# Kernel optimization log

Hardware: AMD Instinct MI355X
Metric: run time of the kernel (lower is better)

Reference implementation:

```python
import jax, jax.numpy as jnp
import numpy as np

N = 50000      # nodes
E = 400000     # edges (before self-loops)
IN = 128
HID = 64
HEADS = 8
OUT = 3
NEG_SLOPE = 0.2
EPS = 1e-6


def setup_inputs() -> dict:
    key = jax.random.key(0)
    ks = jax.random.split(key, 32)
    def nrm(k, shape, s=0.05):
        return jax.random.normal(k, shape, dtype=jnp.float32) * s
    inp = {}
    inp['x'] = nrm(ks[0], (N, IN), 1.0)
    inp['edge_index'] = jax.random.randint(ks[1], (2, E), 0, N)
    inp['res_W'] = nrm(ks[2], (OUT, IN))
    inp['res_b'] = jnp.zeros((OUT,), jnp.float32)
    # (in, out, heads, concat) per GAT layer
    dims = [(IN, HID, HEADS, True), (HID * HEADS, HID, HEADS, True),
            (HID * HEADS, HID, HEADS, True), (HID * HEADS, OUT, 1, False)]
    j = 3
    for i, (ci, co, h, cc) in enumerate(dims):
        inp['ln_g%d' % i] = jnp.ones((ci,), jnp.float32)
        inp['ln_b%d' % i] = jnp.zeros((ci,), jnp.float32)
        inp['W%d' % i] = nrm(ks[j], (h * co, ci)); j += 1
        inp['asr%d' % i] = nrm(ks[j], (h, co)); j += 1
        inp['adt%d' % i] = nrm(ks[j], (h, co)); j += 1
        inp['b%d' % i] = jnp.zeros((h * co if cc else co,), jnp.float32)
    return inp


def layer_norm(x, g, b):
    mu = x.mean(-1, keepdims=True)
    var = ((x - mu) ** 2).mean(-1, keepdims=True)
    return (x - mu) / jnp.sqrt(var + EPS) * g + b


def gat_conv(x, src, dst, W, a_src, a_dst, bias, heads, co, concat):
    n = x.shape[0]
    h = (x @ W.T).reshape(n, heads, co)                    # [N,H,C]
    al_src = jnp.sum(h * a_src, axis=-1)                   # [N,H]
    al_dst = jnp.sum(h * a_dst, axis=-1)                   # [N,H]
    e = jax.nn.leaky_relu(al_src[src] + al_dst[dst], NEG_SLOPE)  # [E',H]
    # segment softmax over incoming edges of each destination node
    m = jax.ops.segment_max(e, dst, num_segments=n)
    e = jnp.exp(e - m[dst])
    s = jax.ops.segment_sum(e, dst, num_segments=n)
    alpha = e / s[dst]                                     # [E',H]
    msg = h[src] * alpha[..., None]                        # [E',H,C]
    out = jax.ops.segment_sum(msg, dst, num_segments=n)    # [N,H,C]
    out = out.reshape(n, heads * co) if concat else out.mean(axis=1)
    return out + bias


def reference(x, edge_index, res_W, res_b,
              ln_g0, ln_b0, W0, asr0, adt0, b0,
              ln_g1, ln_b1, W1, asr1, adt1, b1,
              ln_g2, ln_b2, W2, asr2, adt2, b2,
              ln_g3, ln_b3, W3, asr3, adt3, b3):
    n = x.shape[0]
    loops = jnp.arange(n)
    src = jnp.concatenate([edge_index[0], loops])          # add self-loops (PyG default)
    dst = jnp.concatenate([edge_index[1], loops])
    residual = x @ res_W.T + res_b
    layers = [(ln_g0, ln_b0, W0, asr0, adt0, b0, HEADS, HID, True),
              (ln_g1, ln_b1, W1, asr1, adt1, b1, HEADS, HID, True),
              (ln_g2, ln_b2, W2, asr2, adt2, b2, HEADS, HID, True),
              (ln_g3, ln_b3, W3, asr3, adt3, b3, 1, OUT, False)]
    h = x
    num_layers = len(layers)
    for i, (g, bb, W, a_s, a_d, bi, hd, co, cc) in enumerate(layers):
        x_res = h
        h = layer_norm(h, g, bb)
        h = gat_conv(h, src, dst, W, a_s, a_d, bi, hd, co, cc)
        if i < num_layers - 1:
            h = jax.nn.gelu(h, approximate=False)
            if h.shape == x_res.shape:
                h = h + x_res
    return h + residual
```

## Files before the change

### kernel.cpp

```cpp
#include <hip/hip_runtime.h>
#include <math.h>

#define NN 50000
#define MPAD 50048
#define EE 400000
#define NE 450000
#define IN_F 128
#define NEG_SLOPE 0.2f
#define EPSV 1e-6f

typedef unsigned short bf16u;
typedef short bf8_t __attribute__((ext_vector_type(8)));
typedef float f32x4 __attribute__((ext_vector_type(4)));

__device__ __forceinline__ float bf2f(unsigned int u) {
    return __uint_as_float(u << 16);
}
__device__ __forceinline__ float bf2f_hi(unsigned int u) {
    return __uint_as_float(u & 0xFFFF0000u);
}
__device__ __forceinline__ bf16u f2bf(float f) {
    unsigned int u = __float_as_uint(f);
    unsigned int r = (u + 0x7FFFu + ((u >> 16) & 1u)) >> 16;
    return (bf16u)r;
}
__device__ __forceinline__ float gelu_f(float v) {
    return 0.5f * v * (1.0f + erff(v * 0.70710678118654752f));
}

__device__ __forceinline__ void gload_lds16(const void* g, void* l) {
    __builtin_amdgcn_global_load_lds(
        (__attribute__((address_space(1))) void*)(g),
        (__attribute__((address_space(3))) void*)(l), 16, 0, 0);
}

__global__ void k_zero_i32(int* p, int n) {
    int i = blockIdx.x * 256 + threadIdx.x;
    if (i < n) p[i] = 0;
}

__global__ void k_deg(const int* __restrict__ ei, int* __restrict__ deg) {
    int i = blockIdx.x * 256 + threadIdx.x;
    if (i >= NE) return;
    int d = (i < EE) ? ei[EE + i] : (i - EE);
    atomicAdd(&deg[d], 1);
}

__global__ __launch_bounds__(256) void k_scan1(const int* __restrict__ deg,
                                               int* __restrict__ incl,
                                               int* __restrict__ bsums, int n) {
    __shared__ int sm[1024];
    int base = blockIdx.x * 1024;
    for (int i = threadIdx.x; i < 1024; i += 256)
        sm[i] = (base + i < n) ? deg[base + i] : 0;
    __syncthreads();
    for (int off = 1; off < 1024; off <<= 1) {
        int v[4];
#pragma unroll
        for (int j = 0; j < 4; j++) {
            int i = threadIdx.x + 256 * j;
            v[j] = (i >= off) ? sm[i - off] : 0;
        }
        __syncthreads();
#pragma unroll
        for (int j = 0; j < 4; j++) {
            int i = threadIdx.x + 256 * j;
            sm[i] += v[j];
        }
        __syncthreads();
    }
    for (int i = threadIdx.x; i < 1024; i += 256)
        if (base + i < n) incl[base + i] = sm[i];
    if (threadIdx.x == 0) bsums[blockIdx.x] = sm[1023];
}

__global__ void k_scan2(int* bsums, int nb) {
    if (threadIdx.x == 0 && blockIdx.x == 0) {
        int run = 0;
        for (int i = 0; i < nb; i++) { int v = bsums[i]; bsums[i] = run; run += v; }
    }
}

__global__ void k_scan3(const int* __restrict__ deg, int* __restrict__ rowptr,
                        int* __restrict__ cursor, const int* __restrict__ bsums,
                        int n, int ne) {
    int i = blockIdx.x * 256 + threadIdx.x;
    if (i < n) {
        int excl = rowptr[i] + bsums[i >> 10] - deg[i];
        rowptr[i] = excl;
        cursor[i] = excl;
    }
    if (i == n) rowptr[n] = ne;
}

__global__ void k_scatter(const int* __restrict__ ei, int* __restrict__ cursor,
                          int* __restrict__ col) {
    int i = blockIdx.x * 256 + threadIdx.x;
    if (i >= NE) return;
    int s, d;
    if (i < EE) { s = ei[i]; d = ei[EE + i]; }
    else        { s = i - EE; d = i - EE; }
    int p = atomicAdd(&cursor[d], 1);
    col[p] = s;
}

__global__ void k_cast(const float* __restrict__ x, bf16u* __restrict__ h, int total) {
    int i = blockIdx.x * 256 + threadIdx.x;
    if (i < total) h[i] = f2bf(x[i]);
}

__global__ __launch_bounds__(256) void k_castres(const float* __restrict__ x,
                                                 const float* __restrict__ rw,
                                                 const float* __restrict__ rb,
                                                 bf16u* __restrict__ h,
                                                 float* __restrict__ stats,
                                                 float* __restrict__ res, int n) {
    int row = (blockIdx.x * 256 + threadIdx.x) >> 6;
    int lane = threadIdx.x & 63;
    if (row >= n) return;
    float2 v = *(const float2*)(x + (size_t)row * 128 + lane * 2);
    unsigned int pk = (unsigned int)f2bf(v.x) | ((unsigned int)f2bf(v.y) << 16);
    *(unsigned int*)(h + (size_t)row * 128 + lane * 2) = pk;
    float2 w0 = *(const float2*)(rw + 0 * 128 + lane * 2);
    float2 w1 = *(const float2*)(rw + 1 * 128 + lane * 2);
    float2 w2 = *(const float2*)(rw + 2 * 128 + lane * 2);
    float s = v.x + v.y, s2 = v.x * v.x + v.y * v.y;
    float a0 = v.x * w0.x + v.y * w0.y;
    float a1 = v.x * w1.x + v.y * w1.y;
    float a2 = v.x * w2.x + v.y * w2.y;
#pragma unroll
    for (int off = 32; off; off >>= 1) {
        s  += __shfl_xor(s, off);
        s2 += __shfl_xor(s2, off);
        a0 += __shfl_xor(a0, off);
        a1 += __shfl_xor(a1, off);
        a2 += __shfl_xor(a2, off);
    }
    if (lane == 0) {
        float mu = s * (1.0f / 128.0f);
        float var = s2 * (1.0f / 128.0f) - mu * mu;
        stats[row * 2 + 0] = mu;
        stats[row * 2 + 1] = rsqrtf(var + EPSV);
        res[row * 3 + 0] = a0 + rb[0];
        res[row * 3 + 1] = a1 + rb[1];
        res[row * 3 + 2] = a2 + rb[2];
    }
}

#define BM 128
#define BN 128
#define BKK 32
__global__ __launch_bounds__(256) void k_gemm_mfma(const bf16u* __restrict__ H,
                                                   const float* __restrict__ stats,
                                                   const float* __restrict__ g,
                                                   const float* __restrict__ bbias,
                                                   const bf16u* __restrict__ Wb,
                                                   bf16u* __restrict__ C,
                                                   const float* __restrict__ asr,
                                                   const float* __restrict__ adt,
                                                   float* __restrict__ alsrc,
                                                   float* __restrict__ aldst,
                                                   int Mreal, int ci, int K) {
    __shared__ __align__(16) bf16u As[BM * BKK];
    __shared__ __align__(16) bf16u Bs[BN * BKK];
    const int tid = threadIdx.x;
    const int w = tid >> 6, lane = tid & 63;
    const int row0 = blockIdx.x * BM, col0 = blockIdx.y * BN;
    const int wr = (w >> 1) * 64, wc = (w & 1) * 64;

    const int srow = w * 32 + (lane >> 2);
    const int scol = (lane & 3) * 8;
    const bf16u* gA = H + (size_t)(row0 + srow) * ci + scol;
    const bf16u* gB = Wb + (size_t)(col0 + srow) * ci + scol;
    const float mu1 = stats[(row0 + srow) * 2 + 0];
    const float rs1 = stats[(row0 + srow) * 2 + 1];
    const float mu2 = stats[(row0 + srow + 16) * 2 + 0];
    const float rs2 = stats[(row0 + srow + 16) * 2 + 1];
    bf16u* lA1 = &As[(size_t)srow * BKK + scol];
    bf16u* lA2 = &As[(size_t)(srow + 16) * BKK + scol];
    void* lB1 = &Bs[(size_t)(w * 32) * BKK];
    void* lB2 = &Bs[(size_t)(w * 32 + 16) * BKK];

    f32x4 acc[4][4] = {};

    const int fr = lane & 15;
    const int fk = (lane >> 4) * 8;

    for (int k0 = 0; k0 < ci; k0 += BKK) {
        uint4 ra1 = *(const uint4*)(gA + k0);
        uint4 ra2 = *(const uint4*)(gA + (size_t)16 * ci + k0);
        float4 g0 = *(const float4*)(g + k0 + scol);
        float4 g1 = *(const float4*)(g + k0 + scol + 4);
        float4 b0 = *(const float4*)(bbias + k0 + scol);
        float4 b1 = *(const float4*)(bbias + k0 + scol + 4);
        float gg[8] = {g0.x, g0.y, g0.z, g0.w, g1.x, g1.y, g1.z, g1.w};
        float bb[8] = {b0.x, b0.y, b0.z, b0.w, b1.x, b1.y, b1.z, b1.w};
        unsigned int u1[4] = {ra1.x, ra1.y, ra1.z, ra1.w};
        unsigned int u2[4] = {ra2.x, ra2.y, ra2.z, ra2.w};
        uint4 p1, p2;
        {
            unsigned int po[4], qo[4];
#pragma unroll
            for (int j = 0; j < 4; j++) {
                float va = (bf2f(u1[j] & 0xFFFFu) - mu1) * rs1;
                float vb = (bf2f_hi(u1[j])         - mu1) * rs1;
                float oa = fmaf(va, gg[2 * j], bb[2 * j]);
                float ob = fmaf(vb, gg[2 * j + 1], bb[2 * j + 1]);
                po[j] = (unsigned int)f2bf(oa) | ((unsigned int)f2bf(ob) << 16);
                float vc = (bf2f(u2[j] & 0xFFFFu) - mu2) * rs2;
                float vd = (bf2f_hi(u2[j])         - mu2) * rs2;
                float oc = fmaf(vc, gg[2 * j], bb[2 * j]);
                float od = fmaf(vd, gg[2 * j + 1], bb[2 * j + 1]);
                qo[j] = (unsigned int)f2bf(oc) | ((unsigned int)f2bf(od) << 16);
            }
            p1 = make_uint4(po[0], po[1], po[2], po[3]);
            p2 = make_uint4(qo[0], qo[1], qo[2], qo[3]);
        }

        __syncthreads();
        *(uint4*)lA1 = p1;
        *(uint4*)lA2 = p2;
        gload_lds16(gB + k0, lB1);
        gload_lds16(gB + (size_t)16 * ci + k0, lB2);
        __syncthreads();

        bf8_t af[4], bf[4];
#pragma unroll
        for (int m = 0; m < 4; m++)
            af[m] = *(const bf8_t*)&As[(size_t)(wr + m * 16 + fr) * BKK + fk];
#pragma unroll
        for (int n = 0; n < 4; n++)
            bf[n] = *(const bf8_t*)&Bs[(size_t)(wc + n * 16 + fr) * BKK + fk];
#pragma unroll
        for (int m = 0; m < 4; m++)
#pragma unroll
            for (int n = 0; n < 4; n++)
                acc[m][n] = __builtin_amdgcn_mfma_f32_16x16x32_bf16(af[m], bf[n], acc[m][n], 0, 0, 0);
    }

    const int fc = lane & 15;
    const int fq = (lane >> 4) * 4;

#pragma unroll
    for (int m = 0; m < 4; m++) {
#pragma unroll
        for (int r = 0; r < 4; r++) {
            int row = row0 + wr + m * 16 + fq + r;
            if (row >= Mreal) continue;
#pragma unroll
            for (int n = 0; n < 4; n++) {
                int col = col0 + wc + n * 16 + fc;
                C[(size_t)row * K + col] = f2bf(acc[m][n][r]);
            }
        }
    }

    const int head = blockIdx.y * 2 + (wc >> 6);
    float av[4], dv[4];
#pragma unroll
    for (int n = 0; n < 4; n++) {
        av[n] = asr[head * 64 + n * 16 + fc];
        dv[n] = adt[head * 64 + n * 16 + fc];
    }
#pragma unroll
    for (int m = 0; m < 4; m++) {
#pragma unroll
        for (int r = 0; r < 4; r++) {
            float s1 = acc[m][0][r] * av[0] + acc[m][1][r] * av[1]
                     + acc[m][2][r] * av[2] + acc[m][3][r] * av[3];
            float s2 = acc[m][0][r] * dv[0] + acc[m][1][r] * dv[1]
                     + acc[m][2][r] * dv[2] + acc[m][3][r] * dv[3];
#pragma unroll
            for (int o = 1; o < 16; o <<= 1) {
                s1 += __shfl_xor(s1, o);
                s2 += __shfl_xor(s2, o);
            }
            int row = row0 + wr + m * 16 + fq + r;
            if (fc == 0 && row < Mreal) {
                alsrc[row * 8 + head] = s1;
                aldst[row * 8 + head] = s2;
            }
        }
    }
}

__global__ __launch_bounds__(256) void k_lin3(const bf16u* __restrict__ h,
                                              const float* __restrict__ stats,
                                              const float* __restrict__ g,
                                              const float* __restrict__ bb,
                                              const float* __restrict__ W,
                                              const float* __restrict__ a_s,
                                              const float* __restrict__ a_d,
                                              bf16u* __restrict__ hlin3,
                                              float* __restrict__ alsrc,
                                              float* __restrict__ aldst, int n) {
    int row = (blockIdx.x * 256 + threadIdx.x) >> 6;
    int lane = threadIdx.x & 63;
    if (row >= n) return;
    float mu = stats[row * 2 + 0], rs = stats[row * 2 + 1];
    uint4 r = *(const uint4*)(h + (size_t)row * 512 + lane * 8);
    float4 g0 = *(const float4*)(g + lane * 8);
    float4 g1 = *(const float4*)(g + lane * 8 + 4);
    float4 b0 = *(const float4*)(bb + lane * 8);
    float4 b1 = *(const float4*)(bb + lane * 8 + 4);
    float gg[8] = {g0.x, g0.y, g0.z, g0.w, g1.x, g1.y, g1.z, g1.w};
    float bv[8] = {b0.x, b0.y, b0.z, b0.w, b1.x, b1.y, b1.z, b1.w};
    unsigned int u[4] = {r.x, r.y, r.z, r.w};
    float ln[8];
#pragma unroll
    for (int j = 0; j < 4; j++) {
        ln[2 * j]     = fmaf((bf2f(u[j] & 0xFFFFu) - mu) * rs, gg[2 * j], bv[2 * j]);
        ln[2 * j + 1] = fmaf((bf2f_hi(u[j])         - mu) * rs, gg[2 * j + 1], bv[2 * j + 1]);
    }
    float a0 = 0.f, a1 = 0.f, a2 = 0.f;
#pragma unroll
    for (int j = 0; j < 8; j++) {
        int k = lane * 8 + j;
        a0 += ln[j] * W[k];
        a1 += ln[j] * W[512 + k];
        a2 += ln[j] * W[1024 + k];
    }
#pragma unroll
    for (int off = 32; off; off >>= 1) {
        a0 += __shfl_down(a0, off);
        a1 += __shfl_down(a1, off);
        a2 += __shfl_down(a2, off);
    }
    if (lane == 0) {
        *(unsigned int*)(hlin3 + (size_t)row * 4) =
            (unsigned int)f2bf(a0) | ((unsigned int)f2bf(a1) << 16);
        *(unsigned int*)(hlin3 + (size_t)row * 4 + 2) = (unsigned int)f2bf(a2);
        alsrc[row] = a0 * a_s[0] + a1 * a_s[1] + a2 * a_s[2];
        aldst[row] = a0 * a_d[0] + a1 * a_d[1] + a2 * a_d[2];
    }
}

__global__ __launch_bounds__(256) void k_aggN(const bf16u* __restrict__ hlin,
                                              const float* __restrict__ alsrc,
                                              const float* __restrict__ aldst,
                                              const int* __restrict__ rowptr,
                                              const int* __restrict__ col,
                                              const float* __restrict__ bias,
                                              bf16u* __restrict__ hio,
                                              float* __restrict__ stats,
                                              int n, int dores) {
    __shared__ uint2 aldsU[4][8][66];
    int wv = threadIdx.x >> 6;
    int node = (blockIdx.x * 256 + threadIdx.x) >> 6;
    int lane = threadIdx.x & 63;
    if (node >= n) return;
    int beg = rowptr[node], end = rowptr[node + 1];
    int deg = end - beg;

    const float4* dvv = (const float4*)(aldst + node * 8);
    float4 da = dvv[0], db = dvv[1];
    float ad[8] = {da.x, da.y, da.z, da.w, db.x, db.y, db.z, db.w};

    float s = 0.f, s2 = 0.f;

    if (deg <= 64) {
        unsigned int offb = 0;
        float raw[8];
#pragma unroll
        for (int h = 0; h < 8; h++) raw[h] = -INFINITY;
        if (lane < deg) {
            int srcreg = col[beg + lane];
            offb = (unsigned int)srcreg << 10;
            const float4* sv = (const float4*)(alsrc + srcreg * 8);
            float4 sa = sv[0], sb = sv[1];
            float sl[8] = {sa.x, sa.y, sa.z, sa.w, sb.x, sb.y, sb.z, sb.w};
#pragma unroll
            for (int h = 0; h < 8; h++) {
                float v = sl[h] + ad[h];
                raw[h] = (v >= 0.f) ? v : NEG_SLOPE * v;
            }
        }
        float m[8];
#pragma unroll
        for (int h = 0; h < 8; h++) m[h] = raw[h];
#pragma unroll
        for (int off = 32; off; off >>= 1)
#pragma unroll
            for (int h = 0; h < 8; h++) m[h] = fmaxf(m[h], __shfl_xor(m[h], off));
        float ex[8], sm[8];
#pragma unroll
        for (int h = 0; h < 8; h++) {
            ex[h] = (lane < deg) ? __expf(raw[h] - m[h]) : 0.f;
            sm[h] = ex[h];
        }
#pragma unroll
        for (int off = 32; off; off >>= 1)
#pragma unroll
            for (int h = 0; h < 8; h++) sm[h] += __shfl_xor(sm[h], off);
#pragma unroll
        for (int h = 0; h < 8; h++) {
            uint2 t;
            t.x = __float_as_uint(ex[h] * (1.0f / sm[h]));
            t.y = offb;
            aldsU[wv][h][lane] = t;
        }
        asm volatile("s_waitcnt lgkmcnt(0)" ::: "memory");

        int hl = lane >> 3;
        const uint2* myal = &aldsU[wv][hl][0];
        const char* base2 = (const char*)hlin + (lane << 4);
        float acc[8] = {};
        int e = 0;
        for (; e + 2 <= deg; e += 2) {
            uint2 t0 = myal[e];
            uint2 t1 = myal[e + 1];
            uint4 u0 = *(const uint4*)(base2 + t0.y);
            uint4 u1 = *(const uint4*)(base2 + t1.y);
            float a0 = __uint_as_float(t0.x), a1 = __uint_as_float(t1.x);
            acc[0] = fmaf(a0, bf2f(u0.x & 0xFFFFu), acc[0]);
            acc[1] = fmaf(a0, bf2f_hi(u0.x),        acc[1]);
            acc[2] = fmaf(a0, bf2f(u0.y & 0xFFFFu), acc[2]);
            acc[3] = fmaf(a0, bf2f_hi(u0.y),        acc[3]);
            acc[4] = fmaf(a0, bf2f(u0.z & 0xFFFFu), acc[4]);
            acc[5] = fmaf(a0, bf2f_hi(u0.z),        acc[5]);
            acc[6] = fmaf(a0, bf2f(u0.w & 0xFFFFu), acc[6]);
            acc[7] = fmaf(a0, bf2f_hi(u0.w),        acc[7]);
            acc[0] = fmaf(a1, bf2f(u1.x & 0xFFFFu), acc[0]);
            acc[1] = fmaf(a1, bf2f_hi(u1.x),        acc[1]);
            acc[2] = fmaf(a1, bf2f(u1.y & 0xFFFFu), acc[2]);
            acc[3] = fmaf(a1, bf2f_hi(u1.y),        acc[3]);
            acc[4] = fmaf(a1, bf2f(u1.z & 0xFFFFu), acc[4]);
            acc[5] = fmaf(a1, bf2f_hi(u1.z),        acc[5]);
            acc[6] = fmaf(a1, bf2f(u1.w & 0xFFFFu), acc[6]);
            acc[7] = fmaf(a1, bf2f_hi(u1.w),        acc[7]);
        }
        if (e < deg) {
            uint2 t0 = myal[e];
            uint4 u0 = *(const uint4*)(base2 + t0.y);
            float a0 = __uint_as_float(t0.x);
            acc[0] = fmaf(a0, bf2f(u0.x & 0xFFFFu), acc[0]);
            acc[1] = fmaf(a0, bf2f_hi(u0.x),        acc[1]);
            acc[2] = fmaf(a0, bf2f(u0.y & 0xFFFFu), acc[2]);
            acc[3] = fmaf(a0, bf2f_hi(u0.y),        acc[3]);
            acc[4] = fmaf(a0, bf2f(u0.z & 0xFFFFu), acc[4]);
            acc[5] = fmaf(a0, bf2f_hi(u0.z),        acc[5]);
            acc[6] = fmaf(a0, bf2f(u0.w & 0xFFFFu), acc[6]);
            acc[7] = fmaf(a0, bf2f_hi(u0.w),        acc[7]);
        }

        size_t idx = (size_t)node * 512 + lane * 8;
        float4 b0 = *(const float4*)(bias + lane * 8);
        float4 b1 = *(const float4*)(bias + lane * 8 + 4);
        float bb[8] = {b0.x, b0.y, b0.z, b0.w, b1.x, b1.y, b1.z, b1.w};
        float fin[8];
#pragma unroll
        for (int j = 0; j < 8; j++) fin[j] = gelu_f(acc[j] + bb[j]);
        if (dores) {
            uint4 up = *(const uint4*)(hio + idx);
            fin[0] += bf2f(up.x & 0xFFFFu); fin[1] += bf2f_hi(up.x);
            fin[2] += bf2f(up.y & 0xFFFFu); fin[3] += bf2f_hi(up.y);
            fin[4] += bf2f(up.z & 0xFFFFu); fin[5] += bf2f_hi(up.z);
            fin[6] += bf2f(up.w & 0xFFFFu); fin[7] += bf2f_hi(up.w);
        }
        uint4 pk;
        pk.x = (unsigned int)f2bf(fin[0]) | ((unsigned int)f2bf(fin[1]) << 16);
        pk.y = (unsigned int)f2bf(fin[2]) | ((unsigned int)f2bf(fin[3]) << 16);
        pk.z = (unsigned int)f2bf(fin[4]) | ((unsigned int)f2bf(fin[5]) << 16);
        pk.w = (unsigned int)f2bf(fin[6]) | ((unsigned int)f2bf(fin[7]) << 16);
        *(uint4*)(hio + idx) = pk;
#pragma unroll
        for (int j = 0; j < 8; j++) { s += fin[j]; s2 += fin[j] * fin[j]; }
    } else {
        for (int h = 0; h < 8; h++) {
            float adh = ad[h];
            float m = -INFINITY;
            for (int e = beg + lane; e < end; e += 64) {
                float v = alsrc[col[e] * 8 + h] + adh;
                v = (v >= 0.f) ? v : NEG_SLOPE * v;
                m = fmaxf(m, v);
            }
#pragma unroll
            for (int off = 32; off; off >>= 1) m = fmaxf(m, __shfl_xor(m, off));
            float sum = 0.f;
            for (int e = beg + lane; e < end; e += 64) {
                float v = alsrc[col[e] * 8 + h] + adh;
                v = (v >= 0.f) ? v : NEG_SLOPE * v;
                sum += __expf(v - m);
            }
#pragma unroll
            for (int off = 32; off; off >>= 1) sum += __shfl_xor(sum, off);
            float inv = 1.0f / sum;
            float acc = 0.f;
            for (int e = beg; e < end; e++) {
                int src = col[e];
                float v = alsrc[src * 8 + h] + adh;
                v = (v >= 0.f) ? v : NEG_SLOPE * v;
                float alpha = __expf(v - m) * inv;
                acc = fmaf(alpha, bf2f(hlin[((size_t)src << 9) + h * 64 + lane]), acc);
            }
            float fin = gelu_f(acc + bias[h * 64 + lane]);
            size_t idx = (size_t)node * 512 + h * 64 + lane;
            if (dores) fin += bf2f(hio[idx]);
            hio[idx] = f2bf(fin);
            s += fin; s2 += fin * fin;
        }
    }

#pragma unroll
    for (int off = 32; off; off >>= 1) {
        s  += __shfl_xor(s, off);
        s2 += __shfl_xor(s2, off);
    }
    if (lane == 0) {
        float mu = s * (1.0f / 512.0f);
        float var = s2 * (1.0f / 512.0f) - mu * mu;
        stats[node * 2 + 0] = mu;
        stats[node * 2 + 1] = rsqrtf(var + EPSV);
    }
}

__global__ __launch_bounds__(256) void k_aggF(const bf16u* __restrict__ hlin3,
                                              const float* __restrict__ alsrc,
                                              const float* __restrict__ aldst,
                                              const int* __restrict__ rowptr,
                                              const int* __restrict__ col,
                                              const float* __restrict__ bias,
                                              float* __restrict__ outf,
                                              const float* __restrict__ resid, int n) {
    int node = (blockIdx.x * 256 + threadIdx.x) >> 6;
    int lane = threadIdx.x & 63;
    if (node >= n) return;
    int beg = rowptr[node], end = rowptr[node + 1];
    int deg = end - beg;
    float adh = aldst[node];

    if (deg <= 64) {
        int src = 0;
        float raw = -INFINITY;
        if (lane < deg) {
            src = col[beg + lane];
            float v = alsrc[src] + adh;
            raw = (v >= 0.f) ? v : NEG_SLOPE * v;
        }
        float m = raw;
#pragma unroll
        for (int off = 32; off; off >>= 1) m = fmaxf(m, __shfl_xor(m, off));
        float ex = (lane < deg) ? __expf(raw - m) : 0.f;
        float sum = ex;
#pragma unroll
        for (int off = 32; off; off >>= 1) sum += __shfl_xor(sum, off);
        float alpha = ex / sum;

        float c0 = 0.f, c1 = 0.f, c2 = 0.f;
        if (lane < deg) {
            uint2 u = *(const uint2*)(hlin3 + (size_t)src * 4);
            c0 = alpha * bf2f(u.x & 0xFFFFu);
            c1 = alpha * bf2f_hi(u.x);
            c2 = alpha * bf2f(u.y & 0xFFFFu);
        }
#pragma unroll
        for (int off = 32; off; off >>= 1) {
            c0 += __shfl_xor(c0, off);
            c1 += __shfl_xor(c1, off);
            c2 += __shfl_xor(c2, off);
        }
        if (lane == 0) {
            outf[node * 3 + 0] = c0 + bias[0] + resid[node * 3 + 0];
            outf[node * 3 + 1] = c1 + bias[1] + resid[node * 3 + 1];
            outf[node * 3 + 2] = c2 + bias[2] + resid[node * 3 + 2];
        }
    } else {
        float m = -INFINITY;
        for (int e = beg + lane; e < end; e += 64) {
            float v = alsrc[col[e]] + adh;
            v = (v >= 0.f) ? v : NEG_SLOPE * v;
            m = fmaxf(m, v);
        }
#pragma unroll
        for (int off = 32; off; off >>= 1) m = fmaxf(m, __shfl_xor(m, off));
        float sum = 0.f;
        for (int e = beg + lane; e < end; e += 64) {
            float v = alsrc[col[e]] + adh;
            v = (v >= 0.f) ? v : NEG_SLOPE * v;
            sum += __expf(v - m);
        }
#pragma unroll
        for (int off = 32; off; off >>= 1) sum += __shfl_xor(sum, off);
        float inv = 1.0f / sum;
        float acc = 0.f;
        for (int e = beg; e < end; e++) {
            int src = col[e];
            float v = alsrc[src] + adh;
            v = (v >= 0.f) ? v : NEG_SLOPE * v;
            float alpha = __expf(v - m) * inv;
            if (lane < 3) acc += alpha * bf2f(hlin3[(size_t)src * 4 + lane]);
        }
        if (lane < 3)
            outf[node * 3 + lane] = acc + bias[lane] + resid[node * 3 + lane];
    }
}

extern "C" void kernel_launch(void* const* d_in, const int* in_sizes, int n_in,
                              void* d_out, int out_size, void* d_ws, size_t ws_size,
                              hipStream_t stream) {
    const float* x    = (const float*)d_in[0];
    const int*   ei   = (const int*)d_in[1];
    const float* resW = (const float*)d_in[2];
    const float* resb = (const float*)d_in[3];
    const float *lng[4], *lnb[4], *Wm[4], *asr[4], *adt[4], *bias[4];
    int idx = 4;
    for (int i = 0; i < 4; i++) {
        lng[i]  = (const float*)d_in[idx++];
        lnb[i]  = (const float*)d_in[idx++];
        Wm[i]   = (const float*)d_in[idx++];
        asr[i]  = (const float*)d_in[idx++];
        adt[i]  = (const float*)d_in[idx++];
        bias[i] = (const float*)d_in[idx++];
    }

    char* base = (char*)d_ws;
    size_t off = 0;
    auto alloc = [&](size_t bytes) {
        void* p = base + off;
        off += (bytes + 255) & ~(size_t)255;
        return p;
    };
    bf16u* hbuf  = (bf16u*)alloc((size_t)MPAD * 512 * 2);
    bf16u* lbuf  = (bf16u*)alloc((size_t)MPAD * 512 * 2);
    bf16u* wb0   = (bf16u*)alloc((size_t)512 * 128 * 2);
    bf16u* wb1   = (bf16u*)alloc((size_t)512 * 512 * 2);
    bf16u* wb2   = (bf16u*)alloc((size_t)512 * 512 * 2);
    float* stats = (float*)alloc((size_t)MPAD * 2 * 4);
    float* alsrc = (float*)alloc((size_t)NN * 8 * 4);
    float* aldst = (float*)alloc((size_t)NN * 8 * 4);
    float* resid = (float*)alloc((size_t)NN * 3 * 4);
    int* rowptr  = (int*)alloc((size_t)(NN + 1) * 4);
    int* cursor  = (int*)alloc((size_t)NN * 4);
    int* deg     = (int*)alloc((size_t)NN * 4);
    int* colidx  = (int*)alloc((size_t)NE * 4);
    int* bsums   = (int*)alloc(256 * 4);
    if (off > ws_size) return;

    float* out = (float*)d_out;

    k_zero_i32<<<(NN + 255) / 256, 256, 0, stream>>>(deg, NN);
    k_deg<<<(NE + 255) / 256, 256, 0, stream>>>(ei, deg);
    int nb = (NN + 1023) / 1024;
    k_scan1<<<nb, 256, 0, stream>>>(deg, rowptr, bsums, NN);
    k_scan2<<<1, 64, 0, stream>>>(bsums, nb);
    k_scan3<<<(NN + 1 + 255) / 256, 256, 0, stream>>>(deg, rowptr, cursor, bsums, NN, NE);
    k_scatter<<<(NE + 255) / 256, 256, 0, stream>>>(ei, cursor, colidx);

    int rowBlocks = (NN * 64 + 255) / 256;
    k_castres<<<rowBlocks, 256, 0, stream>>>(x, resW, resb, hbuf, stats, resid, NN);
    k_cast<<<(512 * 128 + 255) / 256, 256, 0, stream>>>(Wm[0], wb0, 512 * 128);
    k_cast<<<(512 * 512 + 255) / 256, 256, 0, stream>>>(Wm[1], wb1, 512 * 512);
    k_cast<<<(512 * 512 + 255) / 256, 256, 0, stream>>>(Wm[2], wb2, 512 * 512);

    const bf16u* wb[3] = {wb0, wb1, wb2};
    const int ci_a[3] = {128, 512, 512};

    for (int i = 0; i < 3; i++) {
        int ci = ci_a[i];
        int dores = (i >= 1) ? 1 : 0;

        dim3 ggrid(MPAD / BM, 512 / BN);
        k_gemm_mfma<<<ggrid, 256, 0, stream>>>(hbuf, stats, lng[i], lnb[i], wb[i],
                                               lbuf, asr[i], adt[i], alsrc, aldst,
                                               NN, ci, 512);

        k_aggN<<<rowBlocks, 256, 0, stream>>>(lbuf, alsrc, aldst, rowptr, colidx,
                                              bias[i], hbuf, stats, NN, dores);
    }

    k_lin3<<<rowBlocks, 256, 0, stream>>>(hbuf, stats, lng[3], lnb[3], Wm[3],
                                          asr[3], adt[3], lbuf, alsrc, aldst, NN);
    k_aggF<<<rowBlocks, 256, 0, stream>>>(lbuf, alsrc, aldst, rowptr, colidx,
                                          bias[3], out, resid, NN);
}
```

Before: 670.1 us.

## Move LayerNorm into aggregation epilogue and use pure swizzled bf16 GEMM

```diff
diff --git a/kernel.cpp b/kernel.cpp
--- a/kernel.cpp
+++ b/kernel.cpp
@@ -141,6 +141,48 @@
         float var = s2 * (1.0f / 128.0f) - mu * mu;
         stats[row * 2 + 0] = mu;
         stats[row * 2 + 1] = rsqrtf(var + EPSV);
+        res[row * 3 + 0] = a0 + rb[0];
+        res[row * 3 + 1] = a1 + rb[1];
+        res[row * 3 + 2] = a2 + rb[2];
+    }
+}
+
+__global__ __launch_bounds__(256) void k_castres2(const float* __restrict__ x,
+                                                  const float* __restrict__ rw,
+                                                  const float* __restrict__ rb,
+                                                  const float* __restrict__ g0,
+                                                  const float* __restrict__ b0,
+                                                  bf16u* __restrict__ abuf,
+                                                  float* __restrict__ res, int n) {
+    int row = (blockIdx.x * 256 + threadIdx.x) >> 6;
+    int lane = threadIdx.x & 63;
+    if (row >= n) return;
+    float2 v = *(const float2*)(x + (size_t)row * 128 + lane * 2);
+    float2 w0 = *(const float2*)(rw + 0 * 128 + lane * 2);
+    float2 w1 = *(const float2*)(rw + 1 * 128 + lane * 2);
+    float2 w2 = *(const float2*)(rw + 2 * 128 + lane * 2);
+    float s = v.x + v.y, s2 = v.x * v.x + v.y * v.y;
+    float a0 = v.x * w0.x + v.y * w0.y;
+    float a1 = v.x * w1.x + v.y * w1.y;
+    float a2 = v.x * w2.x + v.y * w2.y;
+#pragma unroll
+    for (int off = 32; off; off >>= 1) {
+        s  += __shfl_xor(s, off);
+        s2 += __shfl_xor(s2, off);
+        a0 += __shfl_xor(a0, off);
+        a1 += __shfl_xor(a1, off);
+        a2 += __shfl_xor(a2, off);
+    }
+    float mu = s * (1.0f / 128.0f);
+    float var = s2 * (1.0f / 128.0f) - mu * mu;
+    float rs = rsqrtf(var + EPSV);
+    float2 gg = *(const float2*)(g0 + lane * 2);
+    float2 bb = *(const float2*)(b0 + lane * 2);
+    float l0 = fmaf((v.x - mu) * rs, gg.x, bb.x);
+    float l1 = fmaf((v.y - mu) * rs, gg.y, bb.y);
+    *(unsigned int*)(abuf + (size_t)row * 128 + lane * 2) =
+        (unsigned int)f2bf(l0) | ((unsigned int)f2bf(l1) << 16);
+    if (lane == 0) {
         res[row * 3 + 0] = a0 + rb[0];
         res[row * 3 + 1] = a1 + rb[1];
         res[row * 3 + 2] = a2 + rb[2];
@@ -224,18 +266,115 @@
         gload_lds16(gB + (size_t)16 * ci + k0, lB2);
         __syncthreads();
 
-        bf8_t af[4], bf[4];
+        bf8_t af[4], bfv[4];
 #pragma unroll
         for (int m = 0; m < 4; m++)
             af[m] = *(const bf8_t*)&As[(size_t)(wr + m * 16 + fr) * BKK + fk];
 #pragma unroll
         for (int n = 0; n < 4; n++)
-            bf[n] = *(const bf8_t*)&Bs[(size_t)(wc + n * 16 + fr) * BKK + fk];
+            bfv[n] = *(const bf8_t*)&Bs[(size_t)(wc + n * 16 + fr) * BKK + fk];
 #pragma unroll
         for (int m = 0; m < 4; m++)
 #pragma unroll
             for (int n = 0; n < 4; n++)
-                acc[m][n] = __builtin_amdgcn_mfma_f32_16x16x32_bf16(af[m], bf[n], acc[m][n], 0, 0, 0);
+                acc[m][n] = __builtin_amdgcn_mfma_f32_16x16x32_bf16(af[m], bfv[n], acc[m][n], 0, 0, 0);
+    }
+
+    const int fc = lane & 15;
+    const int fq = (lane >> 4) * 4;
+
+#pragma unroll
+    for (int m = 0; m < 4; m++) {
+#pragma unroll
+        for (int r = 0; r < 4; r++) {
+            int row = row0 + wr + m * 16 + fq + r;
+            if (row >= Mreal) continue;
+#pragma unroll
+            for (int n = 0; n < 4; n++) {
+                int col = col0 + wc + n * 16 + fc;
+                C[(size_t)row * K + col] = f2bf(acc[m][n][r]);
+            }
+        }
+    }
+
+    const int head = blockIdx.y * 2 + (wc >> 6);
+    float av[4], dv[4];
+#pragma unroll
+    for (int n = 0; n < 4; n++) {
+        av[n] = asr[head * 64 + n * 16 + fc];
+        dv[n] = adt[head * 64 + n * 16 + fc];
+    }
+#pragma unroll
+    for (int m = 0; m < 4; m++) {
+#pragma unroll
+        for (int r = 0; r < 4; r++) {
+            float s1 = acc[m][0][r] * av[0] + acc[m][1][r] * av[1]
+                     + acc[m][2][r] * av[2] + acc[m][3][r] * av[3];
+            float s2 = acc[m][0][r] * dv[0] + acc[m][1][r] * dv[1]
+                     + acc[m][2][r] * dv[2] + acc[m][3][r] * dv[3];
+#pragma unroll
+            for (int o = 1; o < 16; o <<= 1) {
+                s1 += __shfl_xor(s1, o);
+                s2 += __shfl_xor(s2, o);
+            }
+            int row = row0 + wr + m * 16 + fq + r;
+            if (fc == 0 && row < Mreal) {
+                alsrc[row * 8 + head] = s1;
+                aldst[row * 8 + head] = s2;
+            }
+        }
+    }
+}
+
+#define BK2 64
+__global__ __launch_bounds__(256) void k_gemm_pure(const bf16u* __restrict__ A,
+                                                   const bf16u* __restrict__ Wb,
+                                                   bf16u* __restrict__ C,
+                                                   const float* __restrict__ asr,
+                                                   const float* __restrict__ adt,
+                                                   float* __restrict__ alsrc,
+                                                   float* __restrict__ aldst,
+                                                   int Mreal, int ci, int K) {
+    __shared__ __align__(16) bf16u As[BM * BK2];
+    __shared__ __align__(16) bf16u Bs[BN * BK2];
+    const int tid = threadIdx.x;
+    const int w = tid >> 6, lane = tid & 63;
+    const int row0 = blockIdx.x * BM, col0 = blockIdx.y * BN;
+    const int wr = (w >> 1) * 64, wc = (w & 1) * 64;
+
+    const int lrow = lane >> 3;
+    const int scolx = ((lane & 7) * 8) ^ (lrow << 3);
+    const bf16u* gA = A + (size_t)(row0 + w * 32 + lrow) * ci + scolx;
+    const bf16u* gB = Wb + (size_t)(col0 + w * 32 + lrow) * ci + scolx;
+
+    f32x4 acc[4][4] = {};
+    const int fr = lane & 15;
+    const int fk = (lane >> 4) * 8;
+    const int fxor = (fr & 7) << 3;
+
+    for (int k0 = 0; k0 < ci; k0 += BK2) {
+        __syncthreads();
+#pragma unroll
+        for (int j = 0; j < 4; j++) {
+            gload_lds16(gA + (size_t)(j * 8) * ci + k0, &As[(w * 32 + j * 8) * BK2]);
+            gload_lds16(gB + (size_t)(j * 8) * ci + k0, &Bs[(w * 32 + j * 8) * BK2]);
+        }
+        __syncthreads();
+#pragma unroll
+        for (int ks = 0; ks < 2; ks++) {
+            bf8_t af[4], bfv[4];
+#pragma unroll
+            for (int m = 0; m < 4; m++)
+                af[m] = *(const bf8_t*)&As[(wr + m * 16 + fr) * BK2 + ((ks * 32 + fk) ^ fxor)];
+#pragma unroll
+            for (int n = 0; n < 4; n++)
+                bfv[n] = *(const bf8_t*)&Bs[(wc + n * 16 + fr) * BK2 + ((ks * 32 + fk) ^ fxor)];
+#pragma unroll
+            for (int m = 0; m < 4; m++)
+#pragma unroll
+                for (int n = 0; n < 4; n++)
+                    acc[m][n] = __builtin_amdgcn_mfma_f32_16x16x32_bf16(af[m], bfv[n], acc[m][n], 0, 0, 0);
+        }
     }
 
     const int fc = lane & 15;
@@ -311,6 +450,47 @@
     for (int j = 0; j < 4; j++) {
         ln[2 * j]     = fmaf((bf2f(u[j] & 0xFFFFu) - mu) * rs, gg[2 * j], bv[2 * j]);
         ln[2 * j + 1] = fmaf((bf2f_hi(u[j])         - mu) * rs, gg[2 * j + 1], bv[2 * j + 1]);
+    }
+    float a0 = 0.f, a1 = 0.f, a2 = 0.f;
+#pragma unroll
+    for (int j = 0; j < 8; j++) {
+        int k = lane * 8 + j;
+        a0 += ln[j] * W[k];
+        a1 += ln[j] * W[512 + k];
+        a2 += ln[j] * W[1024 + k];
+    }
+#pragma unroll
+    for (int off = 32; off; off >>= 1) {
+        a0 += __shfl_down(a0, off);
+        a1 += __shfl_down(a1, off);
+        a2 += __shfl_down(a2, off);
+    }
+    if (lane == 0) {
+        *(unsigned int*)(hlin3 + (size_t)row * 4) =
+            (unsigned int)f2bf(a0) | ((unsigned int)f2bf(a1) << 16);
+        *(unsigned int*)(hlin3 + (size_t)row * 4 + 2) = (unsigned int)f2bf(a2);
+        alsrc[row] = a0 * a_s[0] + a1 * a_s[1] + a2 * a_s[2];
+        aldst[row] = a0 * a_d[0] + a1 * a_d[1] + a2 * a_d[2];
+    }
+}
+
+__global__ __launch_bounds__(256) void k_lin3b(const bf16u* __restrict__ an,
+                                               const float* __restrict__ W,
+                                               const float* __restrict__ a_s,
+                                               const float* __restrict__ a_d,
+                                               bf16u* __restrict__ hlin3,
+                                               float* __restrict__ alsrc,
+                                               float* __restrict__ aldst, int n) {
+    int row = (blockIdx.x * 256 + threadIdx.x) >> 6;
+    int lane = threadIdx.x & 63;
+    if (row >= n) return;
+    uint4 r = *(const uint4*)(an + (size_t)row * 512 + lane * 8);
+    unsigned int u[4] = {r.x, r.y, r.z, r.w};
+    float ln[8];
+#pragma unroll
+    for (int j = 0; j < 4; j++) {
+        ln[2 * j]     = bf2f(u[j] & 0xFFFFu);
+        ln[2 * j + 1] = bf2f_hi(u[j]);
     }
     float a0 = 0.f, a1 = 0.f, a2 = 0.f;
 #pragma unroll
@@ -514,6 +694,211 @@
     }
 }
 
+__global__ __launch_bounds__(256) void k_aggN2(const bf16u* __restrict__ hlin,
+                                               const float* __restrict__ alsrc,
+                                               const float* __restrict__ aldst,
+                                               const int* __restrict__ rowptr,
+                                               const int* __restrict__ col,
+                                               const float* __restrict__ bias,
+                                               bf16u* __restrict__ hio,
+                                               const float* __restrict__ gn,
+                                               const float* __restrict__ bn,
+                                               bf16u* __restrict__ abuf,
+                                               int n, int dores) {
+    __shared__ uint2 aldsU[4][8][66];
+    int wv = threadIdx.x >> 6;
+    int node = (blockIdx.x * 256 + threadIdx.x) >> 6;
+    int lane = threadIdx.x & 63;
+    if (node >= n) return;
+    int beg = rowptr[node], end = rowptr[node + 1];
+    int deg = end - beg;
+
+    const float4* dvv = (const float4*)(aldst + node * 8);
+    float4 da = dvv[0], db = dvv[1];
+    float ad[8] = {da.x, da.y, da.z, da.w, db.x, db.y, db.z, db.w};
+
+    float s = 0.f, s2 = 0.f;
+    float fin[8];
+
+    if (deg <= 64) {
+        unsigned int offb = 0;
+        float raw[8];
+#pragma unroll
+        for (int h = 0; h < 8; h++) raw[h] = -INFINITY;
+        if (lane < deg) {
+            int srcreg = col[beg + lane];
+            offb = (unsigned int)srcreg << 10;
+            const float4* sv = (const float4*)(alsrc + srcreg * 8);
+            float4 sa = sv[0], sb = sv[1];
+            float sl[8] = {sa.x, sa.y, sa.z, sa.w, sb.x, sb.y, sb.z, sb.w};
+#pragma unroll
+            for (int h = 0; h < 8; h++) {
+                float v = sl[h] + ad[h];
+                raw[h] = (v >= 0.f) ? v : NEG_SLOPE * v;
+            }
+        }
+        float m[8];
+#pragma unroll
+        for (int h = 0; h < 8; h++) m[h] = raw[h];
+#pragma unroll
+        for (int off = 32; off; off >>= 1)
+#pragma unroll
+            for (int h = 0; h < 8; h++) m[h] = fmaxf(m[h], __shfl_xor(m[h], off));
+        float ex[8], sm[8];
+#pragma unroll
+        for (int h = 0; h < 8; h++) {
+            ex[h] = (lane < deg) ? __expf(raw[h] - m[h]) : 0.f;
+            sm[h] = ex[h];
+        }
+#pragma unroll
+        for (int off = 32; off; off >>= 1)
+#pragma unroll
+            for (int h = 0; h < 8; h++) sm[h] += __shfl_xor(sm[h], off);
+#pragma unroll
+        for (int h = 0; h < 8; h++) {
+            uint2 t;
+            t.x = __float_as_uint(ex[h] * (1.0f / sm[h]));
+            t.y = offb;
+            aldsU[wv][h][lane] = t;
+        }
+        asm volatile("s_waitcnt lgkmcnt(0)" ::: "memory");
+
+        int hl = lane >> 3;
+        const uint2* myal = &aldsU[wv][hl][0];
+        const char* base2 = (const char*)hlin + (lane << 4);
+        float acc[8] = {};
+        int e = 0;
+        for (; e + 2 <= deg; e += 2) {
+            uint2 t0 = myal[e];
+            uint2 t1 = myal[e + 1];
+            uint4 u0 = *(const uint4*)(base2 + t0.y);
+            uint4 u1 = *(const uint4*)(base2 + t1.y);
+            float a0 = __uint_as_float(t0.x), a1 = __uint_as_float(t1.x);
+            acc[0] = fmaf(a0, bf2f(u0.x & 0xFFFFu), acc[0]);
+            acc[1] = fmaf(a0, bf2f_hi(u0.x),        acc[1]);
+            acc[2] = fmaf(a0, bf2f(u0.y & 0xFFFFu), acc[2]);
+            acc[3] = fmaf(a0, bf2f_hi(u0.y),        acc[3]);
+            acc[4] = fmaf(a0, bf2f(u0.z & 0xFFFFu), acc[4]);
+            acc[5] = fmaf(a0, bf2f_hi(u0.z),        acc[5]);
+            acc[6] = fmaf(a0, bf2f(u0.w & 0xFFFFu), acc[6]);
+            acc[7] = fmaf(a0, bf2f_hi(u0.w),        acc[7]);
+            acc[0] = fmaf(a1, bf2f(u1.x & 0xFFFFu), acc[0]);
+            acc[1] = fmaf(a1, bf2f_hi(u1.x),        acc[1]);
+            acc[2] = fmaf(a1, bf2f(u1.y & 0xFFFFu), acc[2]);
+            acc[3] = fmaf(a1, bf2f_hi(u1.y),        acc[3]);
+            acc[4] = fmaf(a1, bf2f(u1.z & 0xFFFFu), acc[4]);
+            acc[5] = fmaf(a1, bf2f_hi(u1.z),        acc[5]);
+            acc[6] = fmaf(a1, bf2f(u1.w & 0xFFFFu), acc[6]);
+            acc[7] = fmaf(a1, bf2f_hi(u1.w),        acc[7]);
+        }
+        if (e < deg) {
+            uint2 t0 = myal[e];
+            uint4 u0 = *(const uint4*)(base2 + t0.y);
+            float a0 = __uint_as_float(t0.x);
+            acc[0] = fmaf(a0, bf2f(u0.x & 0xFFFFu), acc[0]);
+            acc[1] = fmaf(a0, bf2f_hi(u0.x),        acc[1]);
+            acc[2] = fmaf(a0, bf2f(u0.y & 0xFFFFu), acc[2]);
+            acc[3] = fmaf(a0, bf2f_hi(u0.y),        acc[3]);
+            acc[4] = fmaf(a0, bf2f(u0.z & 0xFFFFu), acc[4]);
+            acc[5] = fmaf(a0, bf2f_hi(u0.z),        acc[5]);
+            acc[6] = fmaf(a0, bf2f(u0.w & 0xFFFFu), acc[6]);
+            acc[7] = fmaf(a0, bf2f_hi(u0.w),        acc[7]);
+        }
+
+        size_t idx = (size_t)node * 512 + lane * 8;
+        float4 b0 = *(const float4*)(bias + lane * 8);
+        float4 b1 = *(const float4*)(bias + lane * 8 + 4);
+        float bb[8] = {b0.x, b0.y, b0.z, b0.w, b1.x, b1.y, b1.z, b1.w};
+#pragma unroll
+        for (int j = 0; j < 8; j++) fin[j] = gelu_f(acc[j] + bb[j]);
+        if (dores) {
+            uint4 up = *(const uint4*)(hio + idx);
+            fin[0] += bf2f(up.x & 0xFFFFu); fin[1] += bf2f_hi(up.x);
+            fin[2] += bf2f(up.y & 0xFFFFu); fin[3] += bf2f_hi(up.y);
+            fin[4] += bf2f(up.z & 0xFFFFu); fin[5] += bf2f_hi(up.z);
+            fin[6] += bf2f(up.w & 0xFFFFu); fin[7] += bf2f_hi(up.w);
+        }
+        uint4 pk;
+        pk.x = (unsigned int)f2bf(fin[0]) | ((unsigned int)f2bf(fin[1]) << 16);
+        pk.y = (unsigned int)f2bf(fin[2]) | ((unsigned int)f2bf(fin[3]) << 16);
+        pk.z = (unsigned int)f2bf(fin[4]) | ((unsigned int)f2bf(fin[5]) << 16);
+        pk.w = (unsigned int)f2bf(fin[6]) | ((unsigned int)f2bf(fin[7]) << 16);
+        *(uint4*)(hio + idx) = pk;
+#pragma unroll
+        for (int j = 0; j < 8; j++) { s += fin[j]; s2 += fin[j] * fin[j]; }
+
+#pragma unroll
+        for (int off = 32; off; off >>= 1) {
+            s  += __shfl_xor(s, off);
+            s2 += __shfl_xor(s2, off);
+        }
+        float mu = s * (1.0f / 512.0f);
+        float rs = rsqrtf(s2 * (1.0f / 512.0f) - mu * mu + EPSV);
+        float4 g0 = *(const float4*)(gn + lane * 8);
+        float4 g1 = *(const float4*)(gn + lane * 8 + 4);
+        float4 n0 = *(const float4*)(bn + lane * 8);
+        float4 n1 = *(const float4*)(bn + lane * 8 + 4);
+        float gg[8] = {g0.x, g0.y, g0.z, g0.w, g1.x, g1.y, g1.z, g1.w};
+        float nb[8] = {n0.x, n0.y, n0.z, n0.w, n1.x, n1.y, n1.z, n1.w};
+        float lnv[8];
+#pragma unroll
+        for (int j = 0; j < 8; j++) lnv[j] = fmaf((fin[j] - mu) * rs, gg[j], nb[j]);
+        uint4 pl;
+        pl.x = (unsigned int)f2bf(lnv[0]) | ((unsigned int)f2bf(lnv[1]) << 16);
+        pl.y = (unsigned int)f2bf(lnv[2]) | ((unsigned int)f2bf(lnv[3]) << 16);
+        pl.z = (unsigned int)f2bf(lnv[4]) | ((unsigned int)f2bf(lnv[5]) << 16);
+        pl.w = (unsigned int)f2bf(lnv[6]) | ((unsigned int)f2bf(lnv[7]) << 16);
+        *(uint4*)(abuf + idx) = pl;
+    } else {
+        float fins[8];
+        for (int h = 0; h < 8; h++) {
+            float adh = ad[h];
+            float m = -INFINITY;
+            for (int e = beg + lane; e < end; e += 64) {
+                float v = alsrc[col[e] * 8 + h] + adh;
+                v = (v >= 0.f) ? v : NEG_SLOPE * v;
+                m = fmaxf(m, v);
+            }
+#pragma unroll
+            for (int off = 32; off; off >>= 1) m = fmaxf(m, __shfl_xor(m, off));
+            float sum = 0.f;
+            for (int e = beg + lane; e < end; e += 64) {
+                float v = alsrc[col[e] * 8 + h] + adh;
+                v = (v >= 0.f) ? v : NEG_SLOPE * v;
+                sum += __expf(v - m);
+            }
+#pragma unroll
+            for (int off = 32; off; off >>= 1) sum += __shfl_xor(sum, off);
+            float inv = 1.0f / sum;
+            float acc = 0.f;
+            for (int e = beg; e < end; e++) {
+                int src = col[e];
+                float v = alsrc[src * 8 + h] + adh;
+                v = (v >= 0.f) ? v : NEG_SLOPE * v;
+                float alpha = __expf(v - m) * inv;
+                acc = fmaf(alpha, bf2f(hlin[((size_t)src << 9) + h * 64 + lane]), acc);
+            }
+            float fv = gelu_f(acc + bias[h * 64 + lane]);
+            size_t idx = (size_t)node * 512 + h * 64 + lane;
+            if (dores) fv += bf2f(hio[idx]);
+            hio[idx] = f2bf(fv);
+            fins[h] = fv;
+            s += fv; s2 += fv * fv;
+        }
+#pragma unroll
+        for (int off = 32; off; off >>= 1) {
+            s  += __shfl_xor(s, off);
+            s2 += __shfl_xor(s2, off);
+        }
+        float mu = s * (1.0f / 512.0f);
+        float rs = rsqrtf(s2 * (1.0f / 512.0f) - mu * mu + EPSV);
+        for (int h = 0; h < 8; h++) {
+            int c = h * 64 + lane;
+            abuf[(size_t)node * 512 + c] = f2bf(fmaf((fins[h] - mu) * rs, gn[c], bn[c]));
+        }
+    }
+}
+
 __global__ __launch_bounds__(256) void k_aggF(const bf16u* __restrict__ hlin3,
                                               const float* __restrict__ alsrc,
                                               const float* __restrict__ aldst,
@@ -620,11 +1005,6 @@
         off += (bytes + 255) & ~(size_t)255;
         return p;
     };
-    bf16u* hbuf  = (bf16u*)alloc((size_t)MPAD * 512 * 2);
-    bf16u* lbuf  = (bf16u*)alloc((size_t)MPAD * 512 * 2);
-    bf16u* wb0   = (bf16u*)alloc((size_t)512 * 128 * 2);
-    bf16u* wb1   = (bf16u*)alloc((size_t)512 * 512 * 2);
-    bf16u* wb2   = (bf16u*)alloc((size_t)512 * 512 * 2);
     float* stats = (float*)alloc((size_t)MPAD * 2 * 4);
     float* alsrc = (float*)alloc((size_t)NN * 8 * 4);
     float* aldst = (float*)alloc((size_t)NN * 8 * 4);
@@ -634,7 +1014,15 @@
     int* deg     = (int*)alloc((size_t)NN * 4);
     int* colidx  = (int*)alloc((size_t)NE * 4);
     int* bsums   = (int*)alloc(256 * 4);
-    if (off > ws_size) return;
+    bf16u* wb0   = (bf16u*)alloc((size_t)512 * 128 * 2);
+    bf16u* wb1   = (bf16u*)alloc((size_t)512 * 512 * 2);
+    bf16u* wb2   = (bf16u*)alloc((size_t)512 * 512 * 2);
+    bf16u* hbuf  = (bf16u*)alloc((size_t)MPAD * 512 * 2);
+    bf16u* lbuf  = (bf16u*)alloc((size_t)MPAD * 512 * 2);
+    size_t base_need = off;
+    bf16u* abuf  = (bf16u*)alloc((size_t)MPAD * 512 * 2);
+    int useNew = (off <= ws_size) ? 1 : 0;
+    if (base_need > ws_size) return;
 
     float* out = (float*)d_out;
 
@@ -647,29 +1035,42 @@
     k_scatter<<<(NE + 255) / 256, 256, 0, stream>>>(ei, cursor, colidx);
 
     int rowBlocks = (NN * 64 + 255) / 256;
-    k_castres<<<rowBlocks, 256, 0, stream>>>(x, resW, resb, hbuf, stats, resid, NN);
     k_cast<<<(512 * 128 + 255) / 256, 256, 0, stream>>>(Wm[0], wb0, 512 * 128);
     k_cast<<<(512 * 512 + 255) / 256, 256, 0, stream>>>(Wm[1], wb1, 512 * 512);
     k_cast<<<(512 * 512 + 255) / 256, 256, 0, stream>>>(Wm[2], wb2, 512 * 512);
 
     const bf16u* wb[3] = {wb0, wb1, wb2};
     const int ci_a[3] = {128, 512, 512};
-
-    for (int i = 0; i < 3; i++) {
-        int ci = ci_a[i];
-        int dores = (i >= 1) ? 1 : 0;
-
-        dim3 ggrid(MPAD / BM, 512 / BN);
-        k_gemm_mfma<<<ggrid, 256, 0, stream>>>(hbuf, stats, lng[i], lnb[i], wb[i],
-                                               lbuf, asr[i], adt[i], alsrc, aldst,
-                                               NN, ci, 512);
-
-        k_aggN<<<rowBlocks, 256, 0, stream>>>(lbuf, alsrc, aldst, rowptr, colidx,
-                                              bias[i], hbuf, stats, NN, dores);
-    }
-
-    k_lin3<<<rowBlocks, 256, 0, stream>>>(hbuf, stats, lng[3], lnb[3], Wm[3],
-                                          asr[3], adt[3], lbuf, alsrc, aldst, NN);
+    dim3 ggrid(MPAD / BM, 512 / BN);
+
+    if (useNew) {
+        k_castres2<<<rowBlocks, 256, 0, stream>>>(x, resW, resb, lng[0], lnb[0],
+                                                  abuf, resid, NN);
+        for (int i = 0; i < 3; i++) {
+            int dores = (i >= 1) ? 1 : 0;
+            k_gemm_pure<<<ggrid, 256, 0, stream>>>(abuf, wb[i], lbuf,
+                                                   asr[i], adt[i], alsrc, aldst,
+                                                   NN, ci_a[i], 512);
+            k_aggN2<<<rowBlocks, 256, 0, stream>>>(lbuf, alsrc, aldst, rowptr, colidx,
+                                                   bias[i], hbuf, lng[i + 1], lnb[i + 1],
+                                                   abuf, NN, dores);
+        }
+        k_lin3b<<<rowBlocks, 256, 0, stream>>>(abuf, Wm[3], asr[3], adt[3],
+                                               lbuf, alsrc, aldst, NN);
+    } else {
+        k_castres<<<rowBlocks, 256, 0, stream>>>(x, resW, resb, hbuf, stats, resid, NN);
+        for (int i = 0; i < 3; i++) {
+            int dores = (i >= 1) ? 1 : 0;
+            k_gemm_mfma<<<ggrid, 256, 0, stream>>>(hbuf, stats, lng[i], lnb[i], wb[i],
+                                                   lbuf, asr[i], adt[i], alsrc, aldst,
+                                                   NN, ci_a[i], 512);
+            k_aggN<<<rowBlocks, 256, 0, stream>>>(lbuf, alsrc, aldst, rowptr, colidx,
+                                                  bias[i], hbuf, stats, NN, dores);
+        }
+        k_lin3<<<rowBlocks, 256, 0, stream>>>(hbuf, stats, lng[3], lnb[3], Wm[3],
+                                              asr[3], adt[3], lbuf, alsrc, aldst, NN);
+    }
+
     k_aggF<<<rowBlocks, 256, 0, stream>>>(lbuf, alsrc, aldst, rowptr, colidx,
                                           bias[3], out, resid, NN);
 }
```

New measurement: 666.5 us. No clear change (-0.5%).
